# Optimization experiments

Hardware: AMD Instinct MI355X
Metric: run time of the kernel (lower is better)

The kernel has to match this reference:

```python
import jax, jax.numpy as jnp
import numpy as np

M = 8192      # number of simplices (edges)
F_IN = 32
F_OUT = 32
K1 = 3        # lower Laplacian filter order
K2 = 3        # upper Laplacian filter order


def setup_inputs() -> dict:
    key = jax.random.key(0)
    kx, kl, ku, kw = jax.random.split(key, 4)
    x = jax.random.normal(kx, (M, F_IN), dtype=jnp.float32)
    # scale Laplacians so the Chebyshev recursion stays numerically tame
    scale = 1.0 / np.sqrt(M)
    Ll = jax.random.normal(kl, (M, M), dtype=jnp.float32) * scale
    Lu = jax.random.normal(ku, (M, M), dtype=jnp.float32) * scale
    # xavier-uniform-ish init for W (F_in, F_out, 1+K1+K2)
    gain = np.sqrt(2.0)  # relu gain as in reset_parameters
    bound = gain * np.sqrt(6.0 / (F_IN + F_OUT))
    W = jax.random.uniform(kw, (F_IN, F_OUT, 1 + K1 + K2), dtype=jnp.float32,
                           minval=-bound, maxval=bound)
    return {"x": x, "Ll": Ll, "Lu": Lu, "W": W}


def chebyshev(L, K, x):
    """Chebyshev terms T_1..T_K of L applied to x, stacked on a trailing dim.
    T_0 = x, T_1 = L x, T_k = 2 L T_{k-1} - T_{k-2}. Returns [M, F, K]."""
    t_prev = x
    t_cur = L @ x
    terms = [t_cur]
    for _ in range(K - 1):
        t_next = 2.0 * (L @ t_cur) - t_prev
        t_prev, t_cur = t_cur, t_next
        terms.append(t_cur)
    return jnp.stack(terms, axis=2)


def reference(x, Ll, Lu, W):
    # identity term I @ x == x  -> [M, F_in, 1]
    Ix = x[:, :, None]
    Xl = chebyshev(Ll, K1, x)          # [M, F_in, K1]
    Xu = chebyshev(Lu, K2, x)          # [M, F_in, K2]
    X = jnp.concatenate([Ix, Xl, Xu], axis=2)  # [M, F_in, 1+K1+K2]
    # per-order projection; dropout has p=0.0 so it is the identity
    y = jnp.einsum('nik,iok->no', X, W)        # [M, F_out]
    return y
```

## Files before the change

kernel.cpp:

```cpp
#include <hip/hip_runtime.h>
#include <hip/hip_bf16.h>
#include <stdint.h>

#define Mdim 8192
#define KSTEPS 256

typedef __attribute__((ext_vector_type(8))) short short8v;
typedef __attribute__((ext_vector_type(4))) float f32x4;

static __device__ __forceinline__ short bf16c(float f) {
  __hip_bfloat16 h = __float2bfloat16(f);
  union { __hip_bfloat16 h; short s; } c; c.h = h;
  return c.s;
}

__global__ __launch_bounds__(256)
void convert_repack(const float* __restrict__ src, short* __restrict__ dst)
{
  __shared__ __align__(16) short Lb[16][1032];
  const int tile = blockIdx.x >> 3;
  const int slab = blockIdx.x & 7;
  const int t = threadIdx.x;

  for (int i = 0; i < 16; ++i) {
    const f32x4* p = reinterpret_cast<const f32x4*>(
        src + ((size_t)tile * 16 + i) * Mdim + slab * 1024) + t;
    f32x4 a = __builtin_nontemporal_load(p);
    short* q = &Lb[i][t * 4];
    q[0] = bf16c(a[0]); q[1] = bf16c(a[1]); q[2] = bf16c(a[2]); q[3] = bf16c(a[3]);
  }
  __syncthreads();

  for (int it = 0; it < 8; ++it) {
    const int c = it * 256 + t;
    const int ksl = c >> 6, ln = c & 63;
    short8v v = *reinterpret_cast<const short8v*>(
        &Lb[ln & 15][ksl * 32 + ((ln >> 4) << 3)]);
    reinterpret_cast<short8v*>(dst)[(size_t)(tile * 256 + slab * 32 + ksl) * 64 + ln] = v;
  }
}

__global__ __launch_bounds__(256)
void repack_x(const float* __restrict__ x, short* __restrict__ Bp)
{
  int t = blockIdx.x * 256 + threadIdx.x;
  int l = t & 63, h = (t >> 6) & 1, ks = t >> 7;
  int col = h * 16 + (l & 15);
  int kbase = ks * 32 + ((l >> 4) << 3);
  short8v v;
#pragma unroll
  for (int j = 0; j < 8; ++j) v[j] = bf16c(x[(size_t)(kbase + j) * 32 + col]);
  reinterpret_cast<short8v*>(Bp)[t] = v;
}

template<int HASPREV>
__global__ __launch_bounds__(512)
void gemm_pair(const short* __restrict__ AsL, const short* __restrict__ AsU,
               const short* __restrict__ BpsL, const short* __restrict__ BpsU,
               const float* __restrict__ TprevL, const float* __restrict__ TprevU,
               float* __restrict__ ToutL, float* __restrict__ ToutU,
               short* __restrict__ BpOutL, short* __restrict__ BpOutU)
{
  const int chain = blockIdx.x >> 9;
  const short* As    = chain ? AsU : AsL;
  const short* Bps   = chain ? BpsU : BpsL;
  const float* Tprev = chain ? TprevU : TprevL;
  float* Tout  = chain ? ToutU : ToutL;
  short* BpOut = chain ? BpOutU : BpOutL;

  const int bTile = blockIdx.x & 511;
  const int lane = threadIdx.x & 63;
  const int wid  = threadIdx.x >> 6;
  const int r0 = bTile << 4;
  const int ksbase = wid * 32;

  const short8v* aF = reinterpret_cast<const short8v*>(As)
                      + ((size_t)bTile * 256 + ksbase) * 64 + lane;
  const short8v* bF = reinterpret_cast<const short8v*>(Bps)
                      + (size_t)ksbase * 128 + lane;

  f32x4 acc0 = {0.f, 0.f, 0.f, 0.f};
  f32x4 acc1 = {0.f, 0.f, 0.f, 0.f};

#pragma unroll 8
  for (int ks = 0; ks < 32; ++ks) {
    short8v av = aF[ks * 64];
    short8v b0 = bF[ks * 128];
    short8v b1 = bF[ks * 128 + 64];
    acc0 = __builtin_amdgcn_mfma_f32_16x16x32_bf16(av, b0, acc0, 0, 0, 0);
    acc1 = __builtin_amdgcn_mfma_f32_16x16x32_bf16(av, b1, acc1, 0, 0, 0);
  }

  __shared__ float Cl[8][16][32];
  __shared__ float Cred[16][32];
  {
    const int crow = (lane >> 4) << 2;
    const int ccol = lane & 15;
#pragma unroll
    for (int q = 0; q < 4; ++q) {
      Cl[wid][crow + q][ccol] = acc0[q];
      Cl[wid][crow + q][16 + ccol] = acc1[q];
    }
  }
  __syncthreads();

  {
    const int t = threadIdx.x;
    const int row = t >> 5, col = t & 31;
    float v = Cl[0][row][col] + Cl[1][row][col] + Cl[2][row][col] + Cl[3][row][col]
            + Cl[4][row][col] + Cl[5][row][col] + Cl[6][row][col] + Cl[7][row][col];
    if constexpr (HASPREV) {
      v = 2.f * v - Tprev[(size_t)r0 * 32 + t];
    }
    Tout[(size_t)r0 * 32 + t] = v;
    Cred[row][col] = v;
  }
  __syncthreads();

  if (threadIdx.x < 64) {
    const int t = threadIdx.x;
    const int ksOut = r0 >> 5;
    const int sub = (r0 >> 4) & 1;
    const int h = t >> 5;
    const int lp = (t & 31) + sub * 32;
    const int col = h * 16 + (lp & 15);
    const int lrbase = (lp & 16) ? 8 : 0;
    short8v v;
#pragma unroll
    for (int j = 0; j < 8; ++j) v[j] = bf16c(Cred[lrbase + j][col]);
    reinterpret_cast<short8v*>(BpOut)[(ksOut << 1 | h) * 64 + lp] = v;
  }
}

template<int HASPREV>
__global__ __launch_bounds__(512)
void gemm_f32_stage(const float* __restrict__ Af, const short8v* __restrict__ Bp,
                    const float* __restrict__ Tprev, float* __restrict__ Tout,
                    short* __restrict__ BpOut)
{
  const int lane = threadIdx.x & 63;
  const int wid  = threadIdx.x >> 6;
  const int r0 = blockIdx.x << 4;
  const int arow = r0 + (lane & 15);
  const int koff = (lane >> 4) << 3;
  const int ksbase = wid * 32;

  f32x4 acc0 = {0.f, 0.f, 0.f, 0.f};
  f32x4 acc1 = {0.f, 0.f, 0.f, 0.f};

  const float* ap = Af + (size_t)arow * Mdim + ksbase * 32 + koff;
#pragma unroll 8
  for (int ks = 0; ks < 32; ++ks) {
    const int g = ksbase + ks;
    f32x4 a0 = *reinterpret_cast<const f32x4*>(ap);
    f32x4 a1 = *reinterpret_cast<const f32x4*>(ap + 4);
    short8v av;
#pragma unroll
    for (int j = 0; j < 4; ++j) av[j] = bf16c(a0[j]);
#pragma unroll
    for (int j = 0; j < 4; ++j) av[4 + j] = bf16c(a1[j]);
    short8v b0 = Bp[(g << 1) * 64 + lane];
    short8v b1 = Bp[((g << 1) + 1) * 64 + lane];
    acc0 = __builtin_amdgcn_mfma_f32_16x16x32_bf16(av, b0, acc0, 0, 0, 0);
    acc1 = __builtin_amdgcn_mfma_f32_16x16x32_bf16(av, b1, acc1, 0, 0, 0);
    ap += 32;
  }

  __shared__ float Cl[8][16][32];
  __shared__ float Cred[16][32];
  {
    const int crow = (lane >> 4) << 2;
    const int ccol = lane & 15;
#pragma unroll
    for (int q = 0; q < 4; ++q) {
      Cl[wid][crow + q][ccol] = acc0[q];
      Cl[wid][crow + q][16 + ccol] = acc1[q];
    }
  }
  __syncthreads();
  {
    const int t = threadIdx.x;
    const int row = t >> 5, col = t & 31;
    float v = Cl[0][row][col] + Cl[1][row][col] + Cl[2][row][col] + Cl[3][row][col]
            + Cl[4][row][col] + Cl[5][row][col] + Cl[6][row][col] + Cl[7][row][col];
    if constexpr (HASPREV) {
      v = 2.f * v - Tprev[(size_t)r0 * 32 + t];
    }
    Tout[(size_t)r0 * 32 + t] = v;
    Cred[row][col] = v;
  }
  __syncthreads();
  if (threadIdx.x < 64) {
    const int t = threadIdx.x;
    const int ksOut = r0 >> 5;
    const int sub = (r0 >> 4) & 1;
    const int h = t >> 5;
    const int lp = (t & 31) + sub * 32;
    const int col = h * 16 + (lp & 15);
    const int lrbase = (lp & 16) ? 8 : 0;
    short8v v;
#pragma unroll
    for (int j = 0; j < 8; ++j) v[j] = bf16c(Cred[lrbase + j][col]);
    reinterpret_cast<short8v*>(BpOut)[(ksOut << 1 | h) * 64 + lp] = v;
  }
}

__global__ __launch_bounds__(256)
void combine(const float* __restrict__ x,
             const float* __restrict__ T1l, const float* __restrict__ T2l,
             const float* __restrict__ T3l, const float* __restrict__ T1u,
             const float* __restrict__ T2u, const float* __restrict__ T3u,
             const float* __restrict__ W, float* __restrict__ y)
{
  __shared__ float Wl[7168];
  for (int i = threadIdx.x; i < 7168; i += 256) Wl[i] = W[i];
  __syncthreads();
  int t = blockIdx.x * 256 + threadIdx.x;
  int n = t >> 5, o = t & 31;
  const float* Xs[7] = {x, T1l, T2l, T3l, T1u, T2u, T3u};
  float sum = 0.f;
#pragma unroll
  for (int k = 0; k < 7; ++k) {
    const f32x4* Xr = reinterpret_cast<const f32x4*>(Xs[k] + (size_t)n * 32);
#pragma unroll
    for (int i4 = 0; i4 < 8; ++i4) {
      f32x4 xv = Xr[i4];
#pragma unroll
      for (int j = 0; j < 4; ++j)
        sum += xv[j] * Wl[(i4 * 4 + j) * 224 + o * 7 + k];
    }
  }
  y[t] = sum;
}

extern "C" void kernel_launch(void* const* d_in, const int* in_sizes, int n_in,
                              void* d_out, int out_size, void* d_ws, size_t ws_size,
                              hipStream_t stream)
{
  const float* x  = (const float*)d_in[0];
  const float* Ll = (const float*)d_in[1];
  const float* Lu = (const float*)d_in[2];
  const float* W  = (const float*)d_in[3];
  float* y = (float*)d_out;

  char* ws = (char*)d_ws;
  size_t off = 0;
  auto alloc = [&](size_t bytes) -> void* {
    void* p = ws + off; off += (bytes + 255) & ~(size_t)255; return p;
  };
  short* Bx  = (short*)alloc(512 * 1024);
  short* Bl1 = (short*)alloc(512 * 1024);
  short* Bl2 = (short*)alloc(512 * 1024);
  short* Bu1 = (short*)alloc(512 * 1024);
  short* Bu2 = (short*)alloc(512 * 1024);
  float* T1l = (float*)alloc(1u << 20);
  float* T2l = (float*)alloc(1u << 20);
  float* T3l = (float*)alloc(1u << 20);
  float* T1u = (float*)alloc(1u << 20);
  float* T2u = (float*)alloc(1u << 20);
  float* T3u = (float*)alloc(1u << 20);

  const size_t lbytes = (size_t)Mdim * Mdim * sizeof(short);
  bool useBF = (ws_size >= off + 2 * lbytes);
  short* Llb = nullptr; short* Lub = nullptr;
  if (useBF) { Llb = (short*)alloc(lbytes); Lub = (short*)alloc(lbytes); }

  repack_x<<<128, 256, 0, stream>>>(x, Bx);

  if (useBF) {
    convert_repack<<<4096, 256, 0, stream>>>(Ll, Llb);
    convert_repack<<<4096, 256, 0, stream>>>(Lu, Lub);
    gemm_pair<0><<<1024,512,0,stream>>>(Llb, Lub, Bx,  Bx,  nullptr, nullptr, T1l, T1u, Bl1, Bu1);
    gemm_pair<1><<<1024,512,0,stream>>>(Llb, Lub, Bl1, Bu1, x,       x,       T2l, T2u, Bl2, Bu2);
    gemm_pair<1><<<1024,512,0,stream>>>(Llb, Lub, Bl2, Bu2, T1l,     T1u,     T3l, T3u, Bl1, Bu1);
  } else {
    gemm_f32_stage<0><<<512,512,0,stream>>>(Ll, (const short8v*)Bx,  nullptr, T1l, Bl1);
    gemm_f32_stage<1><<<512,512,0,stream>>>(Ll, (const short8v*)Bl1, x,       T2l, Bl2);
    gemm_f32_stage<1><<<512,512,0,stream>>>(Ll, (const short8v*)Bl2, T1l,     T3l, Bl1);
    gemm_f32_stage<0><<<512,512,0,stream>>>(Lu, (const short8v*)Bx,  nullptr, T1u, Bu1);
    gemm_f32_stage<1><<<512,512,0,stream>>>(Lu, (const short8v*)Bu1, x,       T2u, Bu2);
    gemm_f32_stage<1><<<512,512,0,stream>>>(Lu, (const short8v*)Bu2, T1u,     T3u, Bu1);
  }

  combine<<<1024, 256, 0, stream>>>(x, T1l, T2l, T3l, T1u, T2u, T3u, W, y);
}
```

Measured before the change: 308.0 us.

## Fuse first Chebyshev GEMM into Laplacian conversion and process chains sequentially

The fp32-to-bf16 conversion of each Laplacian now also computes the T1 = L·x product via MFMA while the tile is in shared memory. Per-slab partial sums go to a buffer, and a small reduction kernel produces T1 and its repacked bf16 operand. This removes one full pass over the bf16 Laplacian. The two chains now run one after another through a single bf16 buffer, which halves workspace needs but drops the paired-chain launch and its parallelism. Each later stage launches only 512 blocks, which may lower occupancy.

```diff
diff --git a/kernel.cpp b/kernel.cpp
--- a/kernel.cpp
+++ b/kernel.cpp
@@ -7,6 +7,7 @@
 
 typedef __attribute__((ext_vector_type(8))) short short8v;
 typedef __attribute__((ext_vector_type(4))) float f32x4;
+typedef __attribute__((ext_vector_type(2))) float f32x2;
 
 static __device__ __forceinline__ short bf16c(float f) {
   __hip_bfloat16 h = __float2bfloat16(f);
@@ -15,12 +16,30 @@
 }
 
 __global__ __launch_bounds__(256)
-void convert_repack(const float* __restrict__ src, short* __restrict__ dst)
-{
-  __shared__ __align__(16) short Lb[16][1032];
+void repack_x(const float* __restrict__ x, short* __restrict__ Bp)
+{
+  int t = blockIdx.x * 256 + threadIdx.x;
+  int l = t & 63, h = (t >> 6) & 1, ks = t >> 7;
+  int col = h * 16 + (l & 15);
+  int kbase = ks * 32 + ((l >> 4) << 3);
+  short8v v;
+#pragma unroll
+  for (int j = 0; j < 8; ++j) v[j] = bf16c(x[(size_t)(kbase + j) * 32 + col]);
+  reinterpret_cast<short8v*>(Bp)[t] = v;
+}
+
+__global__ __launch_bounds__(256)
+void convert_t1(const float* __restrict__ src, const short* __restrict__ Bx,
+                short* __restrict__ dst, float* __restrict__ Pt1)
+{
+  __shared__ __align__(16) char sh[16 * 1032 * 2];
+  short (*Lb)[1032] = reinterpret_cast<short (*)[1032]>(sh);
+
   const int tile = blockIdx.x >> 3;
   const int slab = blockIdx.x & 7;
   const int t = threadIdx.x;
+  const int lane = t & 63;
+  const int wid  = t >> 6;
 
   for (int i = 0; i < 16; ++i) {
     const f32x4* p = reinterpret_cast<const f32x4*>(
@@ -31,44 +50,87 @@
   }
   __syncthreads();
 
+  const short8v* bx8 = reinterpret_cast<const short8v*>(Bx);
+  f32x4 acc0 = {0.f, 0.f, 0.f, 0.f};
+  f32x4 acc1 = {0.f, 0.f, 0.f, 0.f};
+#pragma unroll
   for (int it = 0; it < 8; ++it) {
-    const int c = it * 256 + t;
-    const int ksl = c >> 6, ln = c & 63;
-    short8v v = *reinterpret_cast<const short8v*>(
-        &Lb[ln & 15][ksl * 32 + ((ln >> 4) << 3)]);
-    reinterpret_cast<short8v*>(dst)[(size_t)(tile * 256 + slab * 32 + ksl) * 64 + ln] = v;
+    const int ksl = it * 4 + wid;
+    short8v av = *reinterpret_cast<const short8v*>(
+        &Lb[lane & 15][ksl * 32 + ((lane >> 4) << 3)]);
+    reinterpret_cast<short8v*>(dst)[(size_t)(tile * 256 + slab * 32 + ksl) * 64 + lane] = av;
+    const int gks = slab * 32 + ksl;
+    short8v b0 = bx8[(size_t)(gks << 1) * 64 + lane];
+    short8v b1 = bx8[(size_t)((gks << 1) + 1) * 64 + lane];
+    acc0 = __builtin_amdgcn_mfma_f32_16x16x32_bf16(av, b0, acc0, 0, 0, 0);
+    acc1 = __builtin_amdgcn_mfma_f32_16x16x32_bf16(av, b1, acc1, 0, 0, 0);
+  }
+
+  __syncthreads();
+  float* Clf = reinterpret_cast<float*>(sh);
+  {
+    const int crow = (lane >> 4) << 2;
+    const int ccol = lane & 15;
+#pragma unroll
+    for (int q = 0; q < 4; ++q) {
+      Clf[((wid * 16) + crow + q) * 32 + ccol] = acc0[q];
+      Clf[((wid * 16) + crow + q) * 32 + 16 + ccol] = acc1[q];
+    }
+  }
+  __syncthreads();
+  {
+    const int e = t * 2;
+    const int row = e >> 5, col = e & 31;
+    float v0 = Clf[row * 32 + col] + Clf[(16 + row) * 32 + col]
+             + Clf[(32 + row) * 32 + col] + Clf[(48 + row) * 32 + col];
+    float v1 = Clf[row * 32 + col + 1] + Clf[(16 + row) * 32 + col + 1]
+             + Clf[(32 + row) * 32 + col + 1] + Clf[(48 + row) * 32 + col + 1];
+    f32x2 o; o[0] = v0; o[1] = v1;
+    *reinterpret_cast<f32x2*>(Pt1 + (size_t)(tile * 8 + slab) * 512 + e) = o;
   }
 }
 
 __global__ __launch_bounds__(256)
-void repack_x(const float* __restrict__ x, short* __restrict__ Bp)
-{
-  int t = blockIdx.x * 256 + threadIdx.x;
-  int l = t & 63, h = (t >> 6) & 1, ks = t >> 7;
-  int col = h * 16 + (l & 15);
-  int kbase = ks * 32 + ((l >> 4) << 3);
-  short8v v;
-#pragma unroll
-  for (int j = 0; j < 8; ++j) v[j] = bf16c(x[(size_t)(kbase + j) * 32 + col]);
-  reinterpret_cast<short8v*>(Bp)[t] = v;
+void reduce_t1(const float* __restrict__ Pt1, float* __restrict__ Tout,
+               short* __restrict__ BpOut)
+{
+  __shared__ float Cred[16][32];
+  const int tile = blockIdx.x;
+  const int t = threadIdx.x;
+  const int e = t * 2;
+  float s0 = 0.f, s1 = 0.f;
+#pragma unroll
+  for (int s = 0; s < 8; ++s) {
+    f32x2 v = *reinterpret_cast<const f32x2*>(Pt1 + (size_t)(tile * 8 + s) * 512 + e);
+    s0 += v[0]; s1 += v[1];
+  }
+  f32x2 o; o[0] = s0; o[1] = s1;
+  *reinterpret_cast<f32x2*>(Tout + (size_t)tile * 512 + e) = o;
+  Cred[e >> 5][e & 31] = s0;
+  Cred[e >> 5][(e & 31) + 1] = s1;
+  __syncthreads();
+  if (t < 64) {
+    const int r0 = tile << 4;
+    const int ksOut = r0 >> 5;
+    const int sub = (r0 >> 4) & 1;
+    const int h = t >> 5;
+    const int lp = (t & 31) + sub * 32;
+    const int col = h * 16 + (lp & 15);
+    const int lrbase = (lp & 16) ? 8 : 0;
+    short8v v;
+#pragma unroll
+    for (int j = 0; j < 8; ++j) v[j] = bf16c(Cred[lrbase + j][col]);
+    reinterpret_cast<short8v*>(BpOut)[(ksOut << 1 | h) * 64 + lp] = v;
+  }
 }
 
 template<int HASPREV>
 __global__ __launch_bounds__(512)
-void gemm_pair(const short* __restrict__ AsL, const short* __restrict__ AsU,
-               const short* __restrict__ BpsL, const short* __restrict__ BpsU,
-               const float* __restrict__ TprevL, const float* __restrict__ TprevU,
-               float* __restrict__ ToutL, float* __restrict__ ToutU,
-               short* __restrict__ BpOutL, short* __restrict__ BpOutU)
-{
-  const int chain = blockIdx.x >> 9;
-  const short* As    = chain ? AsU : AsL;
-  const short* Bps   = chain ? BpsU : BpsL;
-  const float* Tprev = chain ? TprevU : TprevL;
-  float* Tout  = chain ? ToutU : ToutL;
-  short* BpOut = chain ? BpOutU : BpOutL;
-
-  const int bTile = blockIdx.x & 511;
+void gemm_stage(const short* __restrict__ As, const short* __restrict__ Bps,
+                const float* __restrict__ Tprev, float* __restrict__ Tout,
+                short* __restrict__ BpOut)
+{
+  const int bTile = blockIdx.x;
   const int lane = threadIdx.x & 63;
   const int wid  = threadIdx.x >> 6;
   const int r0 = bTile << 4;
@@ -103,7 +165,6 @@
     }
   }
   __syncthreads();
-
   {
     const int t = threadIdx.x;
     const int row = t >> 5, col = t & 31;
@@ -116,7 +177,6 @@
     Cred[row][col] = v;
   }
   __syncthreads();
-
   if (threadIdx.x < 64) {
     const int t = threadIdx.x;
     const int ksOut = r0 >> 5;
@@ -248,38 +308,40 @@
   auto alloc = [&](size_t bytes) -> void* {
     void* p = ws + off; off += (bytes + 255) & ~(size_t)255; return p;
   };
-  short* Bx  = (short*)alloc(512 * 1024);
-  short* Bl1 = (short*)alloc(512 * 1024);
-  short* Bl2 = (short*)alloc(512 * 1024);
-  short* Bu1 = (short*)alloc(512 * 1024);
-  short* Bu2 = (short*)alloc(512 * 1024);
+  short* Bx = (short*)alloc(512 * 1024);
+  short* B1 = (short*)alloc(512 * 1024);
+  short* B2 = (short*)alloc(512 * 1024);
   float* T1l = (float*)alloc(1u << 20);
   float* T2l = (float*)alloc(1u << 20);
   float* T3l = (float*)alloc(1u << 20);
   float* T1u = (float*)alloc(1u << 20);
   float* T2u = (float*)alloc(1u << 20);
   float* T3u = (float*)alloc(1u << 20);
+  float* Pt1 = (float*)alloc((size_t)512 * 8 * 512 * 4);
 
   const size_t lbytes = (size_t)Mdim * Mdim * sizeof(short);
-  bool useBF = (ws_size >= off + 2 * lbytes);
-  short* Llb = nullptr; short* Lub = nullptr;
-  if (useBF) { Llb = (short*)alloc(lbytes); Lub = (short*)alloc(lbytes); }
+  bool useBF = (ws_size >= off + lbytes);
+  short* Lab = nullptr;
+  if (useBF) Lab = (short*)alloc(lbytes);
 
   repack_x<<<128, 256, 0, stream>>>(x, Bx);
 
   if (useBF) {
-    convert_repack<<<4096, 256, 0, stream>>>(Ll, Llb);
-    convert_repack<<<4096, 256, 0, stream>>>(Lu, Lub);
-    gemm_pair<0><<<1024,512,0,stream>>>(Llb, Lub, Bx,  Bx,  nullptr, nullptr, T1l, T1u, Bl1, Bu1);
-    gemm_pair<1><<<1024,512,0,stream>>>(Llb, Lub, Bl1, Bu1, x,       x,       T2l, T2u, Bl2, Bu2);
-    gemm_pair<1><<<1024,512,0,stream>>>(Llb, Lub, Bl2, Bu2, T1l,     T1u,     T3l, T3u, Bl1, Bu1);
+    convert_t1<<<4096, 256, 0, stream>>>(Ll, Bx, Lab, Pt1);
+    reduce_t1<<<512, 256, 0, stream>>>(Pt1, T1l, B1);
+    gemm_stage<1><<<512, 512, 0, stream>>>(Lab, B1, x,   T2l, B2);
+    gemm_stage<1><<<512, 512, 0, stream>>>(Lab, B2, T1l, T3l, B1);
+    convert_t1<<<4096, 256, 0, stream>>>(Lu, Bx, Lab, Pt1);
+    reduce_t1<<<512, 256, 0, stream>>>(Pt1, T1u, B1);
+    gemm_stage<1><<<512, 512, 0, stream>>>(Lab, B1, x,   T2u, B2);
+    gemm_stage<1><<<512, 512, 0, stream>>>(Lab, B2, T1u, T3u, B1);
   } else {
-    gemm_f32_stage<0><<<512,512,0,stream>>>(Ll, (const short8v*)Bx,  nullptr, T1l, Bl1);
-    gemm_f32_stage<1><<<512,512,0,stream>>>(Ll, (const short8v*)Bl1, x,       T2l, Bl2);
-    gemm_f32_stage<1><<<512,512,0,stream>>>(Ll, (const short8v*)Bl2, T1l,     T3l, Bl1);
-    gemm_f32_stage<0><<<512,512,0,stream>>>(Lu, (const short8v*)Bx,  nullptr, T1u, Bu1);
-    gemm_f32_stage<1><<<512,512,0,stream>>>(Lu, (const short8v*)Bu1, x,       T2u, Bu2);
-    gemm_f32_stage<1><<<512,512,0,stream>>>(Lu, (const short8v*)Bu2, T1u,     T3u, Bu1);
+    gemm_f32_stage<0><<<512,512,0,stream>>>(Ll, (const short8v*)Bx, nullptr, T1l, B1);
+    gemm_f32_stage<1><<<512,512,0,stream>>>(Ll, (const short8v*)B1, x,      T2l, B2);
+    gemm_f32_stage<1><<<512,512,0,stream>>>(Ll, (const short8v*)B2, T1l,    T3l, B1);
+    gemm_f32_stage<0><<<512,512,0,stream>>>(Lu, (const short8v*)Bx, nullptr, T1u, B1);
+    gemm_f32_stage<1><<<512,512,0,stream>>>(Lu, (const short8v*)B1, x,      T2u, B2);
+    gemm_f32_stage<1><<<512,512,0,stream>>>(Lu, (const short8v*)B2, T1u,    T3u, B1);
   }
 
   combine<<<1024, 256, 0, stream>>>(x, T1l, T2l, T3l, T1u, T2u, T3u, W, y);
```

Result: faster. 253.2 us (-17.8%).
